# Performance work log

Hardware: AMD Instinct MI355X
Metric: run time of the kernel (lower is better)

The kernel has to match this reference:

```python
import jax, jax.numpy as jnp
import numpy as np

B, L, E, H = 2, 2048, 1024, 16
D = E // H  # head_dim = 64


def setup_inputs() -> dict:
    key = jax.random.key(0)
    ks = jax.random.split(key, 9)
    s = 1.0 / np.sqrt(E)
    return {
        "query": jax.random.normal(ks[0], (B, L, E), jnp.float32),
        "key": jax.random.normal(ks[1], (B, L, E), jnp.float32),
        "value": jax.random.normal(ks[2], (B, L, E), jnp.float32),
        # torch Linear weights are [out_features, in_features]
        "Wq": jax.random.uniform(ks[3], (E, E), jnp.float32, -s, s),
        "bq": jnp.zeros((E,), jnp.float32),
        "Wk": jax.random.uniform(ks[4], (E, E), jnp.float32, -s, s),  # k_proj, no bias (add_bias_kv=False)
        "Wv": jax.random.uniform(ks[5], (E, E), jnp.float32, -s, s),  # v_proj, no bias
        "Wo": jax.random.uniform(ks[6], (E, E), jnp.float32, -s, s),
        "bo": jnp.zeros((E,), jnp.float32),
    }


def reference(query, key, value, Wq, bq, Wk, Wv, Wo, bo):
    # Projections (torch Linear: y = x @ W.T + b)
    q = query @ Wq.T + bq          # [B, L, E]
    k = key @ Wk.T                 # [B, L, E]
    v = value @ Wv.T               # [B, L, E]
    # Split heads
    q = q.reshape(B, L, H, D)
    k = k.reshape(B, L, H, D)
    v = v.reshape(B, L, H, D)
    # Scaled dot-product attention; the source's chunked online-softmax
    # computes exactly softmax(q k^T / sqrt(D)) v.
    q = q / jnp.sqrt(jnp.asarray(D, q.dtype))
    scores = jnp.einsum("bqhd,bkhd->bhqk", q, k)      # [B, H, L, L]
    probs = jax.nn.softmax(scores, axis=-1)
    out = jnp.einsum("bhqk,bkhd->bqhd", probs, v)     # [B, L, H, D]
    out = out.reshape(B, L, E)
    return out @ Wo.T + bo
```

## Files before the change

kernel.cpp:

```cpp
#include <hip/hip_runtime.h>

typedef __bf16 bf16;
typedef __bf16 bf16x8 __attribute__((ext_vector_type(8)));
typedef __bf16 bf16x4 __attribute__((ext_vector_type(4)));
typedef float  f32x4  __attribute__((ext_vector_type(4)));

#define MFMA_BF16(a, b, c) __builtin_amdgcn_mfma_f32_16x16x32_bf16((a), (b), (c), 0, 0, 0)


__device__ __forceinline__ void async_load16(const bf16* g, const bf16* l) {
    auto gp = (const __attribute__((address_space(1))) unsigned int*)(unsigned long long)(const void*)g;
    auto lp = (__attribute__((address_space(3))) unsigned int*)(unsigned int)(unsigned long long)(const void*)l;
    __builtin_amdgcn_global_load_lds(gp, lp, 16, 0, 0);
}

__global__ void cvt_bf16_kernel(
    const float* __restrict__ s0, const float* __restrict__ s1, const float* __restrict__ s2,
    const float* __restrict__ s3, const float* __restrict__ s4, const float* __restrict__ s5,
    const float* __restrict__ s6,
    bf16* __restrict__ d0, bf16* __restrict__ d1, bf16* __restrict__ d2,
    bf16* __restrict__ d3, bf16* __restrict__ d4, bf16* __restrict__ d5,
    bf16* __restrict__ d6)
{
    unsigned e = (blockIdx.x * 256 + threadIdx.x) * 4;
    const float* src; bf16* dst; unsigned off;
    if (e < 12582912u) {
        unsigned which = e >> 22;
        src = which == 0 ? s0 : (which == 1 ? s1 : s2);
        dst = which == 0 ? d0 : (which == 1 ? d1 : d2);
        off = e & 4194303u;
    } else {
        unsigned ew = e - 12582912u;
        unsigned which = ew >> 20;
        src = which == 0 ? s3 : (which == 1 ? s4 : (which == 2 ? s5 : s6));
        dst = which == 0 ? d3 : (which == 1 ? d4 : (which == 2 ? d5 : d6));
        off = ew & 1048575u;
    }
    float4 f = *(const float4*)(src + off);
    bf16x4 o;
    o.x = (bf16)f.x; o.y = (bf16)f.y; o.z = (bf16)f.z; o.w = (bf16)f.w;
    *(bf16x4*)(dst + off) = o;
}

template<int BN>
__global__ __launch_bounds__(256, (BN == 128) ? 2 : 4) void gemm4_kernel(
    const bf16* __restrict__ Xq, const bf16* __restrict__ Xk, const bf16* __restrict__ Xv,
    const bf16* __restrict__ Ao,
    const bf16* __restrict__ Wq, const bf16* __restrict__ Wk, const bf16* __restrict__ Wv,
    const bf16* __restrict__ Wo,
    const float* __restrict__ bq, const float* __restrict__ bo,
    bf16* __restrict__ Qs, bf16* __restrict__ Ksw, bf16* __restrict__ Vsw,
    float* __restrict__ out, int zbase)
{
    const int z = zbase + blockIdx.z;
    const bf16 *Amat, *Bmat;
    if (z == 0)      { Amat = Wq; Bmat = Xq; }
    else if (z == 1) { Amat = Wk; Bmat = Xk; }
    else if (z == 2) { Amat = Xv; Bmat = Wv; }
    else             { Amat = Wo; Bmat = Ao; }

    const int m0 = (z == 2 ? blockIdx.y : blockIdx.x) * 128;
    const int n0 = (z == 2 ? blockIdx.x : blockIdx.y) * BN;

    __shared__ __align__(16) bf16 lA[128 * 32];
    __shared__ __align__(16) bf16 lB[BN * 32];

    const int tid  = threadIdx.x;
    const int w    = tid >> 6;
    const int lane = tid & 63;
    const int lm   = lane & 15;
    const int g    = lane >> 4;
    const int wm   = (w & 1) * 64;
    const int wn   = (w >> 1) * (BN / 2);
    constexpr int NT = BN / 32;
    constexpr int T  = (128 + BN) / 64;

    f32x4 acc[4][NT] = {};

    for (int kb = 0; kb < 32; kb++) {
        __syncthreads();
#pragma unroll
        for (int t = 0; t < T; t++) {
            int s   = (t * 4 + w) * 64 + lane;
            int row = s >> 2;
            int gs  = s & 3;
            int gg  = gs ^ ((row >> 1) & 3);
            if (row < 128)
                async_load16(Amat + (size_t)(m0 + row) * 1024 + kb * 32 + gg * 8, lA + s * 8);
            else
                async_load16(Bmat + (size_t)(n0 + row - 128) * 1024 + kb * 32 + gg * 8,
                             lB + (s - 512) * 8);
        }
        __syncthreads();

        bf16x8 af[4], bfr[NT];
#pragma unroll
        for (int mt = 0; mt < 4; mt++) {
            int row = wm + mt * 16 + lm;
            af[mt] = *(const bf16x8*)(lA + row * 32 + ((g ^ ((row >> 1) & 3)) << 3));
        }
#pragma unroll
        for (int nt = 0; nt < NT; nt++) {
            int row = wn + nt * 16 + lm;
            bfr[nt] = *(const bf16x8*)(lB + row * 32 + ((g ^ ((row >> 1) & 3)) << 3));
        }
#pragma unroll
        for (int mt = 0; mt < 4; mt++)
#pragma unroll
            for (int nt = 0; nt < NT; nt++)
                acc[mt][nt] = MFMA_BF16(af[mt], bfr[nt], acc[mt][nt]);
    }

    if (z == 3) {
#pragma unroll
        for (int mt = 0; mt < 4; mt++) {
            int mb = m0 + wm + mt * 16 + g * 4;
            f32x4 bov = *(const f32x4*)(bo + mb);
#pragma unroll
            for (int nt = 0; nt < NT; nt++) {
                int n = n0 + wn + nt * 16 + lm;
                f32x4 val;
#pragma unroll
                for (int r = 0; r < 4; r++) val[r] = acc[mt][nt][r] + bov[r];
                *(f32x4*)(out + (size_t)n * 1024 + mb) = val;
            }
        }
    } else if (z == 2) {
#pragma unroll
        for (int mt = 0; mt < 4; mt++) {
            int mb   = m0 + wm + mt * 16 + g * 4;
            int b    = mb >> 11;
            int lpos = mb & 2047;
            int kb2  = lpos >> 6, kc = (lpos >> 5) & 1, gv = (lpos >> 3) & 3, j0 = lpos & 7;
#pragma unroll
            for (int nt = 0; nt < NT; nt++) {
                int n = n0 + wn + nt * 16 + lm;
                int h = n >> 6, mt2 = (n >> 4) & 3, lmv = n & 15;
                bf16x4 ov;
#pragma unroll
                for (int r = 0; r < 4; r++) ov[r] = (bf16)acc[mt][nt][r];
                *(bf16x4*)(Vsw + (size_t)(b * 16 + h) * 131072 +
                           (size_t)((kb2 * 8 + mt2 * 2 + kc) * 64 + gv * 16 + lmv) * 8 + j0) = ov;
            }
        }
    } else if (z == 1) {
#pragma unroll
        for (int mt = 0; mt < 4; mt++) {
            int mb = m0 + wm + mt * 16 + g * 4;
            int h  = mb >> 6;
            int f  = (mb >> 5) & 1, gk = (mb >> 3) & 3, j0 = mb & 7;
#pragma unroll
            for (int nt = 0; nt < NT; nt++) {
                int n    = n0 + wn + nt * 16 + lm;
                int b    = n >> 11;
                int lpos = n & 2047;
                int kb2  = lpos >> 6;
                int rem  = lpos & 63;
                int c    = ((rem >> 4) & 2) | ((rem >> 2) & 1);
                int lmk  = ((rem >> 1) & 12) | (rem & 3);
                bf16x4 ov;
#pragma unroll
                for (int r = 0; r < 4; r++) ov[r] = (bf16)acc[mt][nt][r];
                *(bf16x4*)(Ksw + (size_t)(b * 16 + h) * 131072 +
                           (size_t)((kb2 * 8 + c * 2 + f) * 64 + gk * 16 + lmk) * 8 + j0) = ov;
            }
        }
    } else {
        const float qscale = 0.18033688011112042f;
#pragma unroll
        for (int mt = 0; mt < 4; mt++) {
            int mb  = m0 + wm + mt * 16 + g * 4;
            int h   = mb >> 6;
            int dd0 = mb & 63;
            f32x4 bqv = *(const f32x4*)(bq + mb);
#pragma unroll
            for (int nt = 0; nt < NT; nt++) {
                int n    = n0 + wn + nt * 16 + lm;
                int b    = n >> 11;
                int lpos = n & 2047;
                bf16x4 ov;
#pragma unroll
                for (int r = 0; r < 4; r++)
                    ov[r] = (bf16)((acc[mt][nt][r] + bqv[r]) * qscale);
                *(bf16x4*)(Qs + (size_t)((b * 16 + h) * 2048 + lpos) * 64 + dd0) = ov;
            }
        }
    }
}

__global__ __launch_bounds__(256, 2) void attn_kernel(
    const bf16* __restrict__ Qs, const bf16* __restrict__ Ksw,
    const bf16* __restrict__ Vsw, bf16* __restrict__ attn)
{
    const int tid  = threadIdx.x;
    const int w    = tid >> 6;
    const int lane = tid & 63;
    const int lm   = lane & 15;
    const int g    = lane >> 4;
    const int i    = blockIdx.x;
    const int bh   = ((i & 7) << 2) | ((i >> 3) & 3);
    const int q0   = (i >> 5) * 128 + w * 32;

    const bf16* Qh = Qs  + (size_t)bh * 131072;
    const bf16* Kh = Ksw + (size_t)bh * 131072;
    const bf16* Vh = Vsw + (size_t)bh * 131072;

    __shared__ __align__(16) bf16 kbuf[4096];
    __shared__ __align__(16) bf16 vbuf[4096];
    __shared__ __align__(16) bf16 ost[4][32 * 72];

    bf16x8 qf[2][2];
#pragma unroll
    for (int qi = 0; qi < 2; qi++)
#pragma unroll
        for (int f = 0; f < 2; f++)
            qf[qi][f] = *(const bf16x8*)(Qh + (size_t)(q0 + qi * 16 + lm) * 64 + f * 32 + g * 8);

    const f32x4 fzero = {0.0f, 0.0f, 0.0f, 0.0f};
    f32x4 o[2][4] = {};
    float lsum[2] = {0.0f, 0.0f};

    for (int kb = 0; kb < 32; kb++) {
        __syncthreads();
#pragma unroll
        for (int t = 0; t < 4; t++) {
            int slot = w * 4 + t;
            if (slot < 8)
                async_load16(Kh + ((size_t)(kb * 8 + slot) * 64 + lane) * 8,
                             kbuf + (slot * 64 + lane) * 8);
            else
                async_load16(Vh + ((size_t)(kb * 8 + slot - 8) * 64 + lane) * 8,
                             vbuf + ((slot - 8) * 64 + lane) * 8);
        }
        __syncthreads();

        f32x4 s[2][4];
#pragma unroll
        for (int c = 0; c < 4; c++) {
            bf16x8 kf0 = *(const bf16x8*)(kbuf + ((c * 2 + 0) * 64 + lane) * 8);
            bf16x8 kf1 = *(const bf16x8*)(kbuf + ((c * 2 + 1) * 64 + lane) * 8);
            s[0][c] = MFMA_BF16(kf0, qf[0][0], fzero);
            s[1][c] = MFMA_BF16(kf0, qf[1][0], fzero);
            s[0][c] = MFMA_BF16(kf1, qf[0][1], s[0][c]);
            s[1][c] = MFMA_BF16(kf1, qf[1][1], s[1][c]);
        }

        bf16x8 pb[2][2];
#pragma unroll
        for (int qi = 0; qi < 2; qi++) {
            float part = 0.0f;
#pragma unroll
            for (int kc = 0; kc < 2; kc++)
#pragma unroll
                for (int r = 0; r < 4; r++) {
                    float p0 = __builtin_amdgcn_exp2f(s[qi][2 * kc][r]);
                    float p1 = __builtin_amdgcn_exp2f(s[qi][2 * kc + 1][r]);
                    pb[qi][kc][r]     = (bf16)p0;
                    pb[qi][kc][r + 4] = (bf16)p1;
                    part += p0 + p1;
                }
            lsum[qi] += part;
        }

#pragma unroll
        for (int kc = 0; kc < 2; kc++)
#pragma unroll
            for (int mt = 0; mt < 4; mt++) {
                bf16x8 vf = *(const bf16x8*)(vbuf + ((mt * 2 + kc) * 64 + lane) * 8);
                o[0][mt] = MFMA_BF16(vf, pb[0][kc], o[0][mt]);
                o[1][mt] = MFMA_BF16(vf, pb[1][kc], o[1][mt]);
            }
    }

#pragma unroll
    for (int qi = 0; qi < 2; qi++) {
        lsum[qi] += __shfl_xor(lsum[qi], 16);
        lsum[qi] += __shfl_xor(lsum[qi], 32);
    }

    const int b = bh >> 4, h = bh & 15;
#pragma unroll
    for (int qi = 0; qi < 2; qi++) {
        float inv = 1.0f / lsum[qi];
#pragma unroll
        for (int mt = 0; mt < 4; mt++) {
            bf16x4 ov;
#pragma unroll
            for (int r = 0; r < 4; r++) ov[r] = (bf16)(o[qi][mt][r] * inv);
            *(bf16x4*)(ost[w] + (qi * 16 + lm) * 72 + mt * 16 + g * 4) = ov;
        }
    }
#pragma unroll
    for (int it = 0; it < 4; it++) {
        int cc = it * 64 + lane;
        int q  = cc >> 3, ch = cc & 7;
        bf16x8 t = *(const bf16x8*)(ost[w] + q * 72 + ch * 8);
        *(bf16x8*)(attn + (size_t)(b * 2048 + q0 + q) * 1024 + h * 64 + ch * 8) = t;
    }
}

extern "C" void kernel_launch(void* const* d_in, const int* in_sizes, int n_in,
                              void* d_out, int out_size, void* d_ws, size_t ws_size,
                              hipStream_t stream) {
    const float* query = (const float*)d_in[0];
    const float* key   = (const float*)d_in[1];
    const float* value = (const float*)d_in[2];
    const float* Wq    = (const float*)d_in[3];
    const float* bq    = (const float*)d_in[4];
    const float* Wk    = (const float*)d_in[5];
    const float* Wv    = (const float*)d_in[6];
    const float* Wo    = (const float*)d_in[7];
    const float* bo    = (const float*)d_in[8];

    char* ws = (char*)d_ws;
    bf16* Xq  = (bf16*)(ws);
    bf16* Xk  = (bf16*)(ws + ((size_t)8  << 20));
    bf16* Xv  = (bf16*)(ws + ((size_t)16 << 20));
    bf16* Wqb = (bf16*)(ws + ((size_t)24 << 20));
    bf16* Wkb = (bf16*)(ws + ((size_t)26 << 20));
    bf16* Wvb = (bf16*)(ws + ((size_t)28 << 20));
    bf16* Wob = (bf16*)(ws + ((size_t)30 << 20));
    bf16* Qs  = (bf16*)(ws + ((size_t)32 << 20));
    bf16* Ksw = (bf16*)(ws + ((size_t)40 << 20));
    bf16* Vsw = (bf16*)(ws + ((size_t)48 << 20));
    bf16* attn = Xq;

    cvt_bf16_kernel<<<dim3(16384, 1, 1), 256, 0, stream>>>(
        query, key, value, Wq, Wk, Wv, Wo, Xq, Xk, Xv, Wqb, Wkb, Wvb, Wob);

    gemm4_kernel<128><<<dim3(8, 32, 3), 256, 0, stream>>>(
        Xq, Xk, Xv, attn, Wqb, Wkb, Wvb, Wob, bq, bo, Qs, Ksw, Vsw, (float*)d_out, 0);

    attn_kernel<<<dim3(512, 1, 1), 256, 0, stream>>>(Qs, Ksw, Vsw, attn);

    gemm4_kernel<64><<<dim3(8, 64, 1), 256, 0, stream>>>(
        Xq, Xk, Xv, attn, Wqb, Wkb, Wvb, Wob, bq, bo, Qs, Ksw, Vsw, (float*)d_out, 3);
}
```

Measured before the change: 212.7 us.

## Double-buffer K/V tiles in LDS and prefetch the next block during compute

The attention kernel now keeps two K/V buffers in LDS. Before the loop it loads the first tile, and on each iteration it issues async global-to-LDS loads for the next tile before computing on the current one, so load latency overlaps with the MFMA and exp work. This drops one barrier per iteration. It also raises wave priority around the MFMA sections with s_setprio. In exchange, LDS use per block roughly rises from about 34KB to 50KB, which may limit occupancy, and correctness depends on the end-of-iteration barrier waiting for the outstanding async loads.

```diff
diff --git a/kernel.cpp b/kernel.cpp
--- a/kernel.cpp
+++ b/kernel.cpp
@@ -205,8 +205,8 @@
     const bf16* Kh = Ksw + (size_t)bh * 131072;
     const bf16* Vh = Vsw + (size_t)bh * 131072;
 
-    __shared__ __align__(16) bf16 kbuf[4096];
-    __shared__ __align__(16) bf16 vbuf[4096];
+    __shared__ __align__(16) bf16 kbuf[2][4096];
+    __shared__ __align__(16) bf16 vbuf[2][4096];
     __shared__ __align__(16) bf16 ost[4][32 * 72];
 
     bf16x8 qf[2][2];
@@ -215,35 +215,56 @@
 #pragma unroll
         for (int f = 0; f < 2; f++)
             qf[qi][f] = *(const bf16x8*)(Qh + (size_t)(q0 + qi * 16 + lm) * 64 + f * 32 + g * 8);
+
+#pragma unroll
+    for (int t = 0; t < 4; t++) {
+        int slot = w * 4 + t;
+        if (slot < 8)
+            async_load16(Kh + ((size_t)slot * 64 + lane) * 8,
+                         kbuf[0] + (slot * 64 + lane) * 8);
+        else
+            async_load16(Vh + ((size_t)(slot - 8) * 64 + lane) * 8,
+                         vbuf[0] + ((slot - 8) * 64 + lane) * 8);
+    }
+    __syncthreads();
 
     const f32x4 fzero = {0.0f, 0.0f, 0.0f, 0.0f};
     f32x4 o[2][4] = {};
     float lsum[2] = {0.0f, 0.0f};
 
     for (int kb = 0; kb < 32; kb++) {
-        __syncthreads();
-#pragma unroll
-        for (int t = 0; t < 4; t++) {
-            int slot = w * 4 + t;
-            if (slot < 8)
-                async_load16(Kh + ((size_t)(kb * 8 + slot) * 64 + lane) * 8,
-                             kbuf + (slot * 64 + lane) * 8);
-            else
-                async_load16(Vh + ((size_t)(kb * 8 + slot - 8) * 64 + lane) * 8,
-                             vbuf + ((slot - 8) * 64 + lane) * 8);
-        }
-        __syncthreads();
+        const int cur = kb & 1;
+        const bf16* kcur = kbuf[cur];
+        const bf16* vcur = vbuf[cur];
+
+        if (kb < 31) {
+            bf16* kn = kbuf[cur ^ 1];
+            bf16* vn = vbuf[cur ^ 1];
+#pragma unroll
+            for (int t = 0; t < 4; t++) {
+                int slot = w * 4 + t;
+                if (slot < 8)
+                    async_load16(Kh + ((size_t)((kb + 1) * 8 + slot) * 64 + lane) * 8,
+                                 kn + (slot * 64 + lane) * 8);
+                else
+                    async_load16(Vh + ((size_t)((kb + 1) * 8 + slot - 8) * 64 + lane) * 8,
+                                 vn + ((slot - 8) * 64 + lane) * 8);
+            }
+        }
+        __builtin_amdgcn_sched_barrier(0);
 
         f32x4 s[2][4];
+        __builtin_amdgcn_s_setprio(1);
 #pragma unroll
         for (int c = 0; c < 4; c++) {
-            bf16x8 kf0 = *(const bf16x8*)(kbuf + ((c * 2 + 0) * 64 + lane) * 8);
-            bf16x8 kf1 = *(const bf16x8*)(kbuf + ((c * 2 + 1) * 64 + lane) * 8);
+            bf16x8 kf0 = *(const bf16x8*)(kcur + ((c * 2 + 0) * 64 + lane) * 8);
+            bf16x8 kf1 = *(const bf16x8*)(kcur + ((c * 2 + 1) * 64 + lane) * 8);
             s[0][c] = MFMA_BF16(kf0, qf[0][0], fzero);
             s[1][c] = MFMA_BF16(kf0, qf[1][0], fzero);
             s[0][c] = MFMA_BF16(kf1, qf[0][1], s[0][c]);
             s[1][c] = MFMA_BF16(kf1, qf[1][1], s[1][c]);
         }
+        __builtin_amdgcn_s_setprio(0);
 
         bf16x8 pb[2][2];
 #pragma unroll
@@ -262,14 +283,18 @@
             lsum[qi] += part;
         }
 
+        __builtin_amdgcn_s_setprio(1);
 #pragma unroll
         for (int kc = 0; kc < 2; kc++)
 #pragma unroll
             for (int mt = 0; mt < 4; mt++) {
-                bf16x8 vf = *(const bf16x8*)(vbuf + ((mt * 2 + kc) * 64 + lane) * 8);
+                bf16x8 vf = *(const bf16x8*)(vcur + ((mt * 2 + kc) * 64 + lane) * 8);
                 o[0][mt] = MFMA_BF16(vf, pb[0][kc], o[0][mt]);
                 o[1][mt] = MFMA_BF16(vf, pb[1][kc], o[1][mt]);
             }
+        __builtin_amdgcn_s_setprio(0);
+
+        __syncthreads();
     }
 
 #pragma unroll
```

Result: no change. 213.7 us (+0.4%).

## Load K/V tiles directly into registers with prefetch instead of LDS staging

Applied to the files above, without the earlier changes.

Removes the shared-memory K/V buffers and both per-iteration block barriers. Each wave now loads its K and V fragments straight from global memory into registers, prefetching the next tile after the current one is consumed. It also raises wave priority around the MFMA sections. The cost is that each of the 4 waves loads the full K/V tile itself, roughly quadrupling global/L2 traffic, and register pressure goes up.

```diff
diff --git a/kernel.cpp b/kernel.cpp
--- a/kernel.cpp
+++ b/kernel.cpp
@@ -205,8 +205,6 @@
     const bf16* Kh = Ksw + (size_t)bh * 131072;
     const bf16* Vh = Vsw + (size_t)bh * 131072;
 
-    __shared__ __align__(16) bf16 kbuf[4096];
-    __shared__ __align__(16) bf16 vbuf[4096];
     __shared__ __align__(16) bf16 ost[4][32 * 72];
 
     bf16x8 qf[2][2];
@@ -220,30 +218,33 @@
     f32x4 o[2][4] = {};
     float lsum[2] = {0.0f, 0.0f};
 
+    bf16x8 kf[8], vf[8];
+#pragma unroll
+    for (int t = 0; t < 8; t++)
+        kf[t] = *(const bf16x8*)(Kh + ((size_t)t * 64 + lane) * 8);
+#pragma unroll
+    for (int t = 0; t < 8; t++)
+        vf[t] = *(const bf16x8*)(Vh + ((size_t)t * 64 + lane) * 8);
+
     for (int kb = 0; kb < 32; kb++) {
-        __syncthreads();
-#pragma unroll
-        for (int t = 0; t < 4; t++) {
-            int slot = w * 4 + t;
-            if (slot < 8)
-                async_load16(Kh + ((size_t)(kb * 8 + slot) * 64 + lane) * 8,
-                             kbuf + (slot * 64 + lane) * 8);
-            else
-                async_load16(Vh + ((size_t)(kb * 8 + slot - 8) * 64 + lane) * 8,
-                             vbuf + ((slot - 8) * 64 + lane) * 8);
-        }
-        __syncthreads();
+        const int kn = (kb < 31) ? kb + 1 : 31;
+        const bf16* Kn = Kh + (size_t)kn * 4096;
+        const bf16* Vn = Vh + (size_t)kn * 4096;
 
         f32x4 s[2][4];
+        __builtin_amdgcn_s_setprio(1);
 #pragma unroll
         for (int c = 0; c < 4; c++) {
-            bf16x8 kf0 = *(const bf16x8*)(kbuf + ((c * 2 + 0) * 64 + lane) * 8);
-            bf16x8 kf1 = *(const bf16x8*)(kbuf + ((c * 2 + 1) * 64 + lane) * 8);
-            s[0][c] = MFMA_BF16(kf0, qf[0][0], fzero);
-            s[1][c] = MFMA_BF16(kf0, qf[1][0], fzero);
-            s[0][c] = MFMA_BF16(kf1, qf[0][1], s[0][c]);
-            s[1][c] = MFMA_BF16(kf1, qf[1][1], s[1][c]);
-        }
+            s[0][c] = MFMA_BF16(kf[2 * c],     qf[0][0], fzero);
+            s[1][c] = MFMA_BF16(kf[2 * c],     qf[1][0], fzero);
+            s[0][c] = MFMA_BF16(kf[2 * c + 1], qf[0][1], s[0][c]);
+            s[1][c] = MFMA_BF16(kf[2 * c + 1], qf[1][1], s[1][c]);
+        }
+        __builtin_amdgcn_s_setprio(0);
+
+#pragma unroll
+        for (int t = 0; t < 8; t++)
+            kf[t] = *(const bf16x8*)(Kn + ((size_t)t * 64 + lane) * 8);
 
         bf16x8 pb[2][2];
 #pragma unroll
@@ -262,14 +263,19 @@
             lsum[qi] += part;
         }
 
+        __builtin_amdgcn_s_setprio(1);
 #pragma unroll
         for (int kc = 0; kc < 2; kc++)
 #pragma unroll
             for (int mt = 0; mt < 4; mt++) {
-                bf16x8 vf = *(const bf16x8*)(vbuf + ((mt * 2 + kc) * 64 + lane) * 8);
-                o[0][mt] = MFMA_BF16(vf, pb[0][kc], o[0][mt]);
-                o[1][mt] = MFMA_BF16(vf, pb[1][kc], o[1][mt]);
-            }
+                o[0][mt] = MFMA_BF16(vf[mt * 2 + kc], pb[0][kc], o[0][mt]);
+                o[1][mt] = MFMA_BF16(vf[mt * 2 + kc], pb[1][kc], o[1][mt]);
+            }
+        __builtin_amdgcn_s_setprio(0);
+
+#pragma unroll
+        for (int t = 0; t < 8; t++)
+            vf[t] = *(const bf16x8*)(Vn + ((size_t)t * 64 + lane) * 8);
     }
 
 #pragma unroll
```

Result: no change. 214.6 us (+0.9%).
